# Optimization experiments

Measured on AMD Instinct MI355X. Metric: run time of the kernel, lower is better.

The kernel has to match this reference:

```python
import math
import jax, jax.numpy as jnp
import numpy as np


def setup_inputs() -> dict:
    key = jax.random.key(0)
    k1, k2, k3 = jax.random.split(key, 3)
    n, c, h, w = 4, 128, 64, 64
    return {
        "key": jax.random.normal(k1, (n, c, h, w), dtype=jnp.float32),
        "query": jax.random.normal(k2, (n, c, h, w), dtype=jnp.float32),
        "value": jax.random.normal(k3, (n, c, h, w), dtype=jnp.float32),
    }


def reference(key, query, value):
    n, c, h, w = key.shape
    c2 = value.shape[1]
    hw = h * w
    k = key.reshape(n, c, hw)      # (n, c, hw)
    q = query.reshape(n, c, hw)    # (n, c, hw)
    v = value.reshape(n, c2, hw)   # (n, c2, hw)
    # scores[n, s, t] = sum_c k[n,c,s] * q[n,c,t], scaled by sqrt(c)
    scores = jnp.einsum("ncs,nct->nst", k, q) / math.sqrt(c)
    # softmax over dim=-2 (the key-token axis s)
    p_attn = jax.nn.softmax(scores, axis=-2)
    # p_val[n, e, t] = sum_s v[n,e,s] * p_attn[n,s,t]
    p_val = jnp.einsum("nes,nst->net", v, p_attn)
    return p_val.reshape(n, c2, h, w)
```

## Files before the change

### kernel.cpp

```cpp
#include <hip/hip_runtime.h>


#define HW 4096
#define CC 128
#define KSCALE 0.12751743f
#define CEXP   8.656170245f
#define SMEMB  152576

typedef _Float16 half8  __attribute__((ext_vector_type(8)));
typedef _Float16 half4v __attribute__((ext_vector_type(4)));
typedef float    float4v __attribute__((ext_vector_type(4)));

__device__ __forceinline__ float fast_exp2(float x) {
  return __builtin_amdgcn_exp2f(x);
}

__device__ __forceinline__ void async_copy16(void* lds, const void* g) {
  __builtin_amdgcn_global_load_lds(
      (const __attribute__((address_space(1))) unsigned int*)g,
      (__attribute__((address_space(3))) unsigned int*)lds, 16, 0, 0);
}

__global__ __launch_bounds__(256)
void prepass(const float* __restrict__ K, const float* __restrict__ Q,
             const float* __restrict__ V, _Float16* __restrict__ KT,
             _Float16* __restrict__ QT, _Float16* __restrict__ Vh) {
  const int bid = blockIdx.x;
  const int tid = threadIdx.x;
  if (bid < 2048) {
    __shared__ float tile[32][65];
    const bool isK = bid < 1024;
    const int id = bid & 1023;
    const float* in = isK ? K : Q;
    _Float16* out = isK ? KT : QT;
    const float scale = isK ? KSCALE : 1.0f;
    const int c0 = (id & 3) << 5;
    const int s0 = ((id >> 2) & 63) << 6;
    const int b  = id >> 8;
    const float* ib = in + (size_t)b * CC * HW;
    _Float16* ob = out + (size_t)b * HW * CC;
    const int r  = tid >> 4;
    const int c4 = (tid & 15) * 4;
    *(float4*)&tile[r][c4]      = *(const float4*)(ib + (size_t)(c0 + r) * HW + s0 + c4);
    *(float4*)&tile[r + 16][c4] = *(const float4*)(ib + (size_t)(c0 + r + 16) * HW + s0 + c4);
    __syncthreads();
    const int s  = tid >> 2;
    const int c8 = (tid & 3) * 8;
    half8 h;
    #pragma unroll
    for (int k = 0; k < 8; ++k) h[k] = (_Float16)(tile[c8 + k][s] * scale);
    *(half8*)&ob[(size_t)(s0 + s) * CC + c0 + c8] = h;
  } else {
    const int id = bid - 2048;
    #pragma unroll
    for (int p = 0; p < 4; ++p) {
      const int f = id * 1024 + p * 256 + tid;
      const float4v v = *(const float4v*)(V + 4 * (size_t)f);
      half4v h;
      h.x = (_Float16)v.x; h.y = (_Float16)v.y; h.z = (_Float16)v.z; h.w = (_Float16)v.w;
      *(half4v*)(Vh + 4 * (size_t)f) = h;
    }
  }
}

__global__ __launch_bounds__(512, 4)
void attn_split(const _Float16* __restrict__ KT, const _Float16* __restrict__ QT,
                const _Float16* __restrict__ Vh, float* __restrict__ Opart,
                float* __restrict__ lpart) {
  __shared__ __align__(16) _Float16 sK[2][64][128];
  __shared__ __align__(16) _Float16 sV[2][128][64];
  __shared__ __align__(16) _Float16 sPT[8][16][40];
  __shared__ float sLred[4][2][16];

  const int bid  = blockIdx.x;
  const int xcd  = bid & 7;
  const int idx  = bid >> 3;
  const int half = xcd >> 2;
  const int b    = xcd & 3;
  const int tt0  = idx << 6;
  const int soff = half << 11;
  const int tid  = threadIdx.x;
  const int w    = tid >> 6;
  const int lane = tid & 63;
  const int q    = lane >> 4;
  const int tc   = lane & 15;
  const int g    = w >> 1;
  const int sl   = w & 1;

  const _Float16* KTb = KT + (size_t)b * HW * CC;
  const _Float16* Vb  = Vh + (size_t)b * CC * HW;
  float* Op = Opart + (size_t)(half * 4 + b) * CC * HW;

  half8 qf[4];
  {
    const _Float16* qp = QT + (size_t)b * HW * CC + (size_t)(tt0 + 16 * g + tc) * CC + 8 * q;
    #pragma unroll
    for (int ks = 0; ks < 4; ++ks) qf[ks] = *(const half8*)(qp + 32 * ks);
  }

  const int krow_l = lane >> 4, kchn = lane & 15;
  const int vrow_l = lane >> 3, vchn = lane & 7;
  #define STAGE_S(sn, buf)                                                      \
    {                                                                           \
      _Pragma("unroll")                                                         \
      for (int p = 0; p < 2; ++p) {                                             \
        const int kr = w * 8 + p * 4 + krow_l;                                  \
        const int kg = kchn ^ (kr & 15);                                        \
        async_copy16(&sK[buf][w * 8 + p * 4][0],                                \
                     KTb + (size_t)(soff + (sn) + kr) * CC + kg * 8);           \
        const int vr = w * 16 + p * 8 + vrow_l;                                 \
        const int vg = vchn ^ (vr & 7);                                         \
        async_copy16(&sV[buf][w * 16 + p * 8][0],                               \
                     Vb + (size_t)vr * HW + soff + (sn) + vg * 8);              \
      }                                                                         \
    }

  STAGE_S(0, 0);

  float4v accO[8];
  #pragma unroll
  for (int i2 = 0; i2 < 8; ++i2) accO[i2] = (float4v){0.f, 0.f, 0.f, 0.f};
  float l_part = 0.0f;

  __syncthreads();

  for (int it = 0; it < 2048 / 64; ++it) {
    const int buf = it & 1;
    if (it + 1 < 2048 / 64) STAGE_S((it + 1) * 64, buf ^ 1);

    float4v acc[2];
    acc[0] = (float4v){0.f, 0.f, 0.f, 0.f};
    acc[1] = (float4v){0.f, 0.f, 0.f, 0.f};
    #pragma unroll
    for (int ks = 0; ks < 4; ++ks) {
      #pragma unroll
      for (int j = 0; j < 2; ++j) {
        const int row = 32 * sl + 16 * j + tc;
        const half8 a = *(const half8*)&sK[buf][row][((4 * ks + q) ^ tc) * 8];
        acc[j] = __builtin_amdgcn_mfma_f32_16x16x32_f16(a, qf[ks], acc[j], 0, 0, 0);
      }
    }

    #pragma unroll
    for (int j = 0; j < 2; ++j) {
      const float p0 = fast_exp2(acc[j].x - CEXP);
      const float p1 = fast_exp2(acc[j].y - CEXP);
      const float p2 = fast_exp2(acc[j].z - CEXP);
      const float p3 = fast_exp2(acc[j].w - CEXP);
      l_part += (p0 + p1) + (p2 + p3);
      half4v h;
      h.x = (_Float16)p0; h.y = (_Float16)p1; h.z = (_Float16)p2; h.w = (_Float16)p3;
      *(half4v*)&sPT[w][tc][16 * j + 4 * q] = h;
    }

    const half8 bp = *(const half8*)&sPT[w][tc][8 * q];
    #pragma unroll
    for (int i2 = 0; i2 < 8; ++i2) {
      const half8 av = *(const half8*)&sV[buf][16 * i2 + tc][(((4 * sl + q) ^ (tc & 7))) * 8];
      accO[i2] = __builtin_amdgcn_mfma_f32_16x16x32_f16(av, bp, accO[i2], 0, 0, 0);
    }

    __syncthreads();
  }

  l_part += __shfl_xor(l_part, 16);
  l_part += __shfl_xor(l_part, 32);
  if (lane < 16) sLred[g][sl][tc] = l_part;

  float* mbuf = (float*)&sK[0][0][0];
  if (sl == 1) {
    #pragma unroll
    for (int i2 = 0; i2 < 8; ++i2)
      *(float4v*)&mbuf[g * 2048 + tc * 128 + 16 * i2 + 4 * q] = accO[i2];
  }
  __syncthreads();
  if (sl == 0) {
    const int t = tt0 + 16 * g + tc;
    if (lane < 16) lpart[(size_t)(half * 4 + b) * HW + t] = sLred[g][0][tc] + sLred[g][1][tc];
    #pragma unroll
    for (int i2 = 0; i2 < 8; ++i2) {
      const float4v o = *(const float4v*)&mbuf[g * 2048 + tc * 128 + 16 * i2 + 4 * q];
      const int e0 = 16 * i2 + 4 * q;
      Op[(size_t)(e0 + 0) * HW + t] = accO[i2].x + o.x;
      Op[(size_t)(e0 + 1) * HW + t] = accO[i2].y + o.y;
      Op[(size_t)(e0 + 2) * HW + t] = accO[i2].z + o.z;
      Op[(size_t)(e0 + 3) * HW + t] = accO[i2].w + o.w;
    }
  }
}

__global__ __launch_bounds__(256)
void merge_split(const float* __restrict__ Op, const float* __restrict__ lp,
                 float* __restrict__ out) {
  const int f   = blockIdx.x * 256 + threadIdx.x;
  const int row = f >> 10;
  const int t4  = (f & 1023) << 2;
  const int b   = row >> 7;
  const float4v oa = *(const float4v*)(Op + (size_t)row * HW + t4);
  const float4v ob = *(const float4v*)(Op + ((size_t)row + 512) * HW + t4);
  const float4v la = *(const float4v*)(lp + (size_t)b * HW + t4);
  const float4v lb = *(const float4v*)(lp + ((size_t)b + 4) * HW + t4);
  float4v o;
  o.x = (oa.x + ob.x) / (la.x + lb.x);
  o.y = (oa.y + ob.y) / (la.y + lb.y);
  o.z = (oa.z + ob.z) / (la.z + lb.z);
  o.w = (oa.w + ob.w) / (la.w + lb.w);
  *(float4v*)(out + (size_t)row * HW + t4) = o;
}

__device__ __forceinline__ _Float16* pK(char* s, int buf, int row) {
  return (_Float16*)s + ((size_t)buf * 128 + row) * 128;
}
__device__ __forceinline__ _Float16* pV(char* s, int buf, int row) {
  return (_Float16*)(s + 65536) + ((size_t)buf * 128 + row) * 128;
}
__device__ __forceinline__ _Float16* pP(char* s, int w, int t) {
  return (_Float16*)(s + 131072) + ((size_t)w * 16 + t) * 40;
}
__device__ __forceinline__ float* pL(char* s, int g, int sl) {
  return (float*)(s + 151552) + ((size_t)g * 4 + sl) * 16;
}

__global__ __launch_bounds__(1024, 4)
void attn_mfma(const _Float16* __restrict__ KT, const _Float16* __restrict__ QT,
               const _Float16* __restrict__ Vh, float* __restrict__ Og) {
  __shared__ __align__(16) char smem[SMEMB];
  const int bid = blockIdx.x, tid = threadIdx.x;
  const int b    = bid >> 6;
  const int tt0  = (bid & 63) << 6;
  const int w    = tid >> 6;
  const int lane = tid & 63;
  const int q    = lane >> 4;
  const int tc   = lane & 15;
  const int g    = w >> 2;
  const int sl   = w & 3;

  const _Float16* KTb = KT + (size_t)b * HW * CC;
  const _Float16* Vb  = Vh + (size_t)b * CC * HW;
  float* Ob = Og + (size_t)b * CC * HW;

  half8 qf[4];
  {
    const _Float16* qp = QT + (size_t)b * HW * CC + (size_t)(tt0 + 16 * g + tc) * CC + 8 * q;
    #pragma unroll
    for (int ks = 0; ks < 4; ++ks) qf[ks] = *(const half8*)(qp + 32 * ks);
  }

  const int r0    = w * 8;
  const int lrow  = lane >> 4;
  const int lchnk = lane & 15;
  auto STAGE = [&](int sn, int buf) {
    #pragma unroll
    for (int p = 0; p < 2; ++p) {
      const int row = r0 + p * 4 + lrow;
      const int gc  = lchnk ^ (row & 15);
      async_copy16(pK(smem, buf, r0 + p * 4), KTb + (size_t)(sn + row) * CC + gc * 8);
      async_copy16(pV(smem, buf, r0 + p * 4), Vb + (size_t)row * HW + sn + gc * 8);
    }
  };

  STAGE(0, 0);

  float4v accO[8];
  #pragma unroll
  for (int i2 = 0; i2 < 8; ++i2) accO[i2] = (float4v){0.f, 0.f, 0.f, 0.f};
  float l_part = 0.0f;

  __syncthreads();

  for (int it = 0; it < HW / 128; ++it) {
    const int buf = it & 1;
    if (it + 1 < HW / 128) STAGE((it + 1) * 128, buf ^ 1);

    float4v acc[2];
    acc[0] = (float4v){0.f, 0.f, 0.f, 0.f};
    acc[1] = (float4v){0.f, 0.f, 0.f, 0.f};
    #pragma unroll
    for (int ks = 0; ks < 4; ++ks) {
      #pragma unroll
      for (int j = 0; j < 2; ++j) {
        const int row = 32 * sl + 16 * j + tc;
        const half8 a = *(const half8*)(pK(smem, buf, row) + ((4 * ks + q) ^ tc) * 8);
        acc[j] = __builtin_amdgcn_mfma_f32_16x16x32_f16(a, qf[ks], acc[j], 0, 0, 0);
      }
    }

    #pragma unroll
    for (int j = 0; j < 2; ++j) {
      const float p0 = fast_exp2(acc[j].x - CEXP);
      const float p1 = fast_exp2(acc[j].y - CEXP);
      const float p2 = fast_exp2(acc[j].z - CEXP);
      const float p3 = fast_exp2(acc[j].w - CEXP);
      l_part += (p0 + p1) + (p2 + p3);
      half4v h;
      h.x = (_Float16)p0; h.y = (_Float16)p1; h.z = (_Float16)p2; h.w = (_Float16)p3;
      *(half4v*)(pP(smem, w, tc) + 16 * j + 4 * q) = h;
    }

    const half8 bp = *(const half8*)(pP(smem, w, tc) + 8 * q);
    #pragma unroll
    for (int i2 = 0; i2 < 8; ++i2) {
      const half8 av = *(const half8*)(pV(smem, buf, 16 * i2 + tc) + ((4 * sl + q) ^ tc) * 8);
      accO[i2] = __builtin_amdgcn_mfma_f32_16x16x32_f16(av, bp, accO[i2], 0, 0, 0);
    }

    __syncthreads();
  }

  l_part += __shfl_xor(l_part, 16);
  l_part += __shfl_xor(l_part, 32);
  if (lane < 16) pL(smem, g, sl)[tc] = l_part;

  float* mbuf = (float*)smem;
  if (sl != 0) {
    #pragma unroll
    for (int i2 = 0; i2 < 8; ++i2) {
      const int c4s = (4 * i2 + q) ^ ((tc & 7) << 2);
      *(float4v*)&mbuf[(size_t)(sl - 1) * 8192 + g * 2048 + tc * 128 + 4 * c4s] = accO[i2];
    }
  }
  __syncthreads();
  if (sl == 0) {
    const float li = 1.0f / (((pL(smem, g, 0)[tc] + pL(smem, g, 1)[tc]) +
                              (pL(smem, g, 2)[tc] + pL(smem, g, 3)[tc])));
    const int t = tt0 + 16 * g + tc;
    #pragma unroll
    for (int i2 = 0; i2 < 8; ++i2) {
      const int c4s = (4 * i2 + q) ^ ((tc & 7) << 2);
      float4v o = accO[i2];
      #pragma unroll
      for (int r = 0; r < 3; ++r) {
        const float4v m = *(const float4v*)&mbuf[(size_t)r * 8192 + g * 2048 + tc * 128 + 4 * c4s];
        o.x += m.x; o.y += m.y; o.z += m.z; o.w += m.w;
      }
      const int e0 = 16 * i2 + 4 * q;
      Ob[(size_t)(e0 + 0) * HW + t] = o.x * li;
      Ob[(size_t)(e0 + 1) * HW + t] = o.y * li;
      Ob[(size_t)(e0 + 2) * HW + t] = o.z * li;
      Ob[(size_t)(e0 + 3) * HW + t] = o.w * li;
    }
  }
}

extern "C" void kernel_launch(void* const* d_in, const int* in_sizes, int n_in,
                              void* d_out, int out_size, void* d_ws, size_t ws_size,
                              hipStream_t stream) {
  const float* key   = (const float*)d_in[0];
  const float* query = (const float*)d_in[1];
  const float* value = (const float*)d_in[2];
  float* out = (float*)d_out;

  const size_t TEN   = (size_t)4 * HW * CC * sizeof(_Float16);
  const size_t OPART = (size_t)2 * 4 * CC * HW * sizeof(float);
  const size_t LPART = (size_t)2 * 4 * HW * sizeof(float);
  _Float16* KT = (_Float16*)d_ws;
  _Float16* QT = (_Float16*)((char*)d_ws + TEN);
  _Float16* Vh = (_Float16*)((char*)d_ws + 2 * TEN);
  float* Opart = (float*)((char*)d_ws + 3 * TEN);
  float* lpart = (float*)((char*)d_ws + 3 * TEN + OPART);

  prepass<<<dim3(2560), dim3(256), 0, stream>>>(key, query, value, KT, QT, Vh);
  if (ws_size >= 3 * TEN + OPART + LPART) {
    attn_split<<<dim3(512), dim3(512), 0, stream>>>(KT, QT, Vh, Opart, lpart);
    merge_split<<<dim3(2048), dim3(256), 0, stream>>>(Opart, lpart, out);
  } else {
    attn_mfma<<<dim3(256), dim3(1024), 0, stream>>>(KT, QT, Vh, out);
  }
}
```

Before: 127.8 us.

## Keep attention probabilities in registers and split key rows across waves

Reassigns the wave work split so each wave handles 16 key rows for 32 query tokens, sharing one K fragment across two MFMAs. Exponentiated scores stay in registers and feed a 16x16x16 MFMA directly, which removes the sPT LDS round trip. The cost of this layout is a cross-wave reduction of the output accumulators: partial sums from four waves are combined through staged LDS passes with more barriers. Each wave also holds twice as many accumulator registers, which may limit occupancy.

```diff
diff --git a/kernel.cpp b/kernel.cpp
--- a/kernel.cpp
+++ b/kernel.cpp
@@ -69,8 +69,7 @@
                 float* __restrict__ lpart) {
   __shared__ __align__(16) _Float16 sK[2][64][128];
   __shared__ __align__(16) _Float16 sV[2][128][64];
-  __shared__ __align__(16) _Float16 sPT[8][16][40];
-  __shared__ float sLred[4][2][16];
+  __shared__ float sLred[2][4][32];
 
   const int bid  = blockIdx.x;
   const int xcd  = bid & 7;
@@ -84,18 +83,22 @@
   const int lane = tid & 63;
   const int q    = lane >> 4;
   const int tc   = lane & 15;
-  const int g    = w >> 1;
-  const int sl   = w & 1;
+  const int g2   = w & 1;
+  const int u    = w >> 1;
 
   const _Float16* KTb = KT + (size_t)b * HW * CC;
   const _Float16* Vb  = Vh + (size_t)b * CC * HW;
   float* Op = Opart + (size_t)(half * 4 + b) * CC * HW;
 
-  half8 qf[4];
+  half8 qf[2][4];
   {
-    const _Float16* qp = QT + (size_t)b * HW * CC + (size_t)(tt0 + 16 * g + tc) * CC + 8 * q;
-    #pragma unroll
-    for (int ks = 0; ks < 4; ++ks) qf[ks] = *(const half8*)(qp + 32 * ks);
+    const _Float16* qb = QT + (size_t)b * HW * CC;
+    #pragma unroll
+    for (int f = 0; f < 2; ++f) {
+      const _Float16* qp = qb + (size_t)(tt0 + 32 * g2 + 16 * f + tc) * CC + 8 * q;
+      #pragma unroll
+      for (int ks = 0; ks < 4; ++ks) qf[f][ks] = *(const half8*)(qp + 32 * ks);
+    }
   }
 
   const int krow_l = lane >> 4, kchn = lane & 15;
@@ -117,10 +120,13 @@
 
   STAGE_S(0, 0);
 
-  float4v accO[8];
+  float4v accO[8][2];
   #pragma unroll
-  for (int i2 = 0; i2 < 8; ++i2) accO[i2] = (float4v){0.f, 0.f, 0.f, 0.f};
-  float l_part = 0.0f;
+  for (int i2 = 0; i2 < 8; ++i2) {
+    accO[i2][0] = (float4v){0.f, 0.f, 0.f, 0.f};
+    accO[i2][1] = (float4v){0.f, 0.f, 0.f, 0.f};
+  }
+  float lf0 = 0.0f, lf1 = 0.0f;
 
   __syncthreads();
 
@@ -128,63 +134,95 @@
     const int buf = it & 1;
     if (it + 1 < 2048 / 64) STAGE_S((it + 1) * 64, buf ^ 1);
 
-    float4v acc[2];
-    acc[0] = (float4v){0.f, 0.f, 0.f, 0.f};
-    acc[1] = (float4v){0.f, 0.f, 0.f, 0.f};
+    float4v acc0 = (float4v){0.f, 0.f, 0.f, 0.f};
+    float4v acc1 = (float4v){0.f, 0.f, 0.f, 0.f};
     #pragma unroll
     for (int ks = 0; ks < 4; ++ks) {
-      #pragma unroll
-      for (int j = 0; j < 2; ++j) {
-        const int row = 32 * sl + 16 * j + tc;
-        const half8 a = *(const half8*)&sK[buf][row][((4 * ks + q) ^ tc) * 8];
-        acc[j] = __builtin_amdgcn_mfma_f32_16x16x32_f16(a, qf[ks], acc[j], 0, 0, 0);
-      }
-    }
-
-    #pragma unroll
-    for (int j = 0; j < 2; ++j) {
-      const float p0 = fast_exp2(acc[j].x - CEXP);
-      const float p1 = fast_exp2(acc[j].y - CEXP);
-      const float p2 = fast_exp2(acc[j].z - CEXP);
-      const float p3 = fast_exp2(acc[j].w - CEXP);
-      l_part += (p0 + p1) + (p2 + p3);
-      half4v h;
-      h.x = (_Float16)p0; h.y = (_Float16)p1; h.z = (_Float16)p2; h.w = (_Float16)p3;
-      *(half4v*)&sPT[w][tc][16 * j + 4 * q] = h;
-    }
-
-    const half8 bp = *(const half8*)&sPT[w][tc][8 * q];
+      const half8 a = *(const half8*)&sK[buf][16 * u + tc][((4 * ks + q) ^ tc) * 8];
+      acc0 = __builtin_amdgcn_mfma_f32_16x16x32_f16(a, qf[0][ks], acc0, 0, 0, 0);
+      acc1 = __builtin_amdgcn_mfma_f32_16x16x32_f16(a, qf[1][ks], acc1, 0, 0, 0);
+    }
+
+    half4v pa0, pa1;
+    {
+      const float p0 = fast_exp2(acc0.x - CEXP);
+      const float p1 = fast_exp2(acc0.y - CEXP);
+      const float p2 = fast_exp2(acc0.z - CEXP);
+      const float p3 = fast_exp2(acc0.w - CEXP);
+      lf0 += (p0 + p1) + (p2 + p3);
+      pa0.x = (_Float16)p0; pa0.y = (_Float16)p1; pa0.z = (_Float16)p2; pa0.w = (_Float16)p3;
+    }
+    {
+      const float p0 = fast_exp2(acc1.x - CEXP);
+      const float p1 = fast_exp2(acc1.y - CEXP);
+      const float p2 = fast_exp2(acc1.z - CEXP);
+      const float p3 = fast_exp2(acc1.w - CEXP);
+      lf1 += (p0 + p1) + (p2 + p3);
+      pa1.x = (_Float16)p0; pa1.y = (_Float16)p1; pa1.z = (_Float16)p2; pa1.w = (_Float16)p3;
+    }
+
     #pragma unroll
     for (int i2 = 0; i2 < 8; ++i2) {
-      const half8 av = *(const half8*)&sV[buf][16 * i2 + tc][(((4 * sl + q) ^ (tc & 7))) * 8];
-      accO[i2] = __builtin_amdgcn_mfma_f32_16x16x32_f16(av, bp, accO[i2], 0, 0, 0);
-    }
-
-    __syncthreads();
-  }
-
-  l_part += __shfl_xor(l_part, 16);
-  l_part += __shfl_xor(l_part, 32);
-  if (lane < 16) sLred[g][sl][tc] = l_part;
-
-  float* mbuf = (float*)&sK[0][0][0];
-  if (sl == 1) {
-    #pragma unroll
-    for (int i2 = 0; i2 < 8; ++i2)
-      *(float4v*)&mbuf[g * 2048 + tc * 128 + 16 * i2 + 4 * q] = accO[i2];
-  }
-  __syncthreads();
-  if (sl == 0) {
-    const int t = tt0 + 16 * g + tc;
-    if (lane < 16) lpart[(size_t)(half * 4 + b) * HW + t] = sLred[g][0][tc] + sLred[g][1][tc];
-    #pragma unroll
-    for (int i2 = 0; i2 < 8; ++i2) {
-      const float4v o = *(const float4v*)&mbuf[g * 2048 + tc * 128 + 16 * i2 + 4 * q];
-      const int e0 = 16 * i2 + 4 * q;
-      Op[(size_t)(e0 + 0) * HW + t] = accO[i2].x + o.x;
-      Op[(size_t)(e0 + 1) * HW + t] = accO[i2].y + o.y;
-      Op[(size_t)(e0 + 2) * HW + t] = accO[i2].z + o.z;
-      Op[(size_t)(e0 + 3) * HW + t] = accO[i2].w + o.w;
+      const half4v av = *(const half4v*)
+          &sV[buf][16 * i2 + tc][(((2 * u + (q >> 1)) ^ (tc & 7)) << 3) + ((q & 1) << 2)];
+      accO[i2][0] = __builtin_amdgcn_mfma_f32_16x16x16f16(av, pa0, accO[i2][0], 0, 0, 0);
+      accO[i2][1] = __builtin_amdgcn_mfma_f32_16x16x16f16(av, pa1, accO[i2][1], 0, 0, 0);
+    }
+
+    __syncthreads();
+  }
+
+  lf0 += __shfl_xor(lf0, 16); lf0 += __shfl_xor(lf0, 32);
+  lf1 += __shfl_xor(lf1, 16); lf1 += __shfl_xor(lf1, 32);
+  if (lane < 16) { sLred[g2][u][tc] = lf0; sLred[g2][u][16 + tc] = lf1; }
+
+  float* mb = g2 ? (float*)&sV[0][0][0] : (float*)&sK[0][0][0];
+
+  #pragma unroll
+  for (int f = 0; f < 2; ++f) {
+    __syncthreads();
+    if (u & 1) {
+      float* slot = mb + (u >> 1) * 2112;
+      #pragma unroll
+      for (int i2 = 0; i2 < 8; ++i2)
+        *(float4v*)&slot[tc * 132 + 16 * i2 + 4 * q] = accO[i2][f];
+    }
+    __syncthreads();
+    if (u == 0) {
+      #pragma unroll
+      for (int i2 = 0; i2 < 8; ++i2) {
+        const float4v m = *(const float4v*)&mb[tc * 132 + 16 * i2 + 4 * q];
+        accO[i2][f].x += m.x; accO[i2][f].y += m.y;
+        accO[i2][f].z += m.z; accO[i2][f].w += m.w;
+      }
+    } else if (u == 2) {
+      float* slot = mb + 2112;
+      #pragma unroll
+      for (int i2 = 0; i2 < 8; ++i2) {
+        float4v m = *(const float4v*)&slot[tc * 132 + 16 * i2 + 4 * q];
+        m.x += accO[i2][f].x; m.y += accO[i2][f].y;
+        m.z += accO[i2][f].z; m.w += accO[i2][f].w;
+        *(float4v*)&slot[tc * 132 + 16 * i2 + 4 * q] = m;
+      }
+    }
+    __syncthreads();
+    if (u == 0) {
+      const int t = tt0 + 32 * g2 + 16 * f + tc;
+      if (f == 0 && lane < 32) {
+        const int fl = lane >> 4, tcc = lane & 15;
+        lpart[(size_t)(half * 4 + b) * HW + tt0 + 32 * g2 + 16 * fl + tcc] =
+            (sLred[g2][0][16 * fl + tcc] + sLred[g2][1][16 * fl + tcc]) +
+            (sLred[g2][2][16 * fl + tcc] + sLred[g2][3][16 * fl + tcc]);
+      }
+      #pragma unroll
+      for (int i2 = 0; i2 < 8; ++i2) {
+        const float4v m = *(const float4v*)&mb[2112 + tc * 132 + 16 * i2 + 4 * q];
+        const int e0 = 16 * i2 + 4 * q;
+        Op[(size_t)(e0 + 0) * HW + t] = accO[i2][f].x + m.x;
+        Op[(size_t)(e0 + 1) * HW + t] = accO[i2][f].y + m.y;
+        Op[(size_t)(e0 + 2) * HW + t] = accO[i2][f].z + m.z;
+        Op[(size_t)(e0 + 3) * HW + t] = accO[i2][f].w + m.w;
+      }
     }
   }
 }
```

New measurement: 157.7 us. 23.4% more time.

## Split key axis four ways with smaller tiles and pipelined PV

Applied to the files above, without the earlier changes.

Adds a new attention kernel that splits the key-token axis into four chunks instead of two, launching 1024 blocks with smaller 32-row K/V tiles and 8 blocks per CU occupancy target. The PV matmul for the previous tile is overlapped with the next score computation, and V staging uses a new swizzle. A new merge kernel sums four partials. This aims for more parallelism and occupancy but doubles partial-output traffic to workspace and merge cost.

```diff
diff --git a/kernel.cpp b/kernel.cpp
--- a/kernel.cpp
+++ b/kernel.cpp
@@ -63,6 +63,167 @@
   }
 }
 
+__global__ __launch_bounds__(512, 8)
+void attn_q4(const _Float16* __restrict__ KT, const _Float16* __restrict__ QT,
+             const _Float16* __restrict__ Vh, float* __restrict__ Opart,
+             float* __restrict__ lpart) {
+  __shared__ __align__(16) _Float16 sK[2][32][128];
+  __shared__ __align__(16) _Float16 sV[2][128][32];
+  __shared__ __align__(16) _Float16 sPT[4][16][40];
+  __shared__ float sLred[4][2][16];
+
+  const int bid = blockIdx.x;
+  const int xcd = bid & 7;
+  const int idx = bid >> 3;
+  const int grp = xcd + 8 * (idx >> 6);
+  const int q4  = grp >> 2;
+  const int b   = grp & 3;
+  const int tt0 = (idx & 63) << 6;
+  const int soff = q4 << 10;
+  const int tid  = threadIdx.x;
+  const int w    = tid >> 6;
+  const int lane = tid & 63;
+  const int q    = lane >> 4;
+  const int tc   = lane & 15;
+  const int g    = w >> 1;
+  const int sh   = w & 1;
+
+  const _Float16* KTb = KT + (size_t)b * HW * CC;
+  const _Float16* Vb  = Vh + (size_t)b * CC * HW;
+  float* Op = Opart + (size_t)(q4 * 4 + b) * CC * HW;
+
+  half8 qf[4];
+  {
+    const _Float16* qp = QT + (size_t)b * HW * CC + (size_t)(tt0 + 16 * g + tc) * CC + 8 * q;
+    #pragma unroll
+    for (int ks = 0; ks < 4; ++ks) qf[ks] = *(const half8*)(qp + 32 * ks);
+  }
+
+  const int krow_l = lane >> 4, kchn = lane & 15;
+  const int vrow_l = lane >> 2, vchn = lane & 3;
+  #define STAGE_K(sn, bufn)                                                     \
+    {                                                                           \
+      const int kr = w * 4 + krow_l;                                            \
+      const int kg = kchn ^ (kr & 15);                                          \
+      async_copy16(&sK[bufn][w * 4][0],                                         \
+                   KTb + (size_t)(soff + (sn) + kr) * CC + kg * 8);             \
+    }
+  #define STAGE_V(sn, bufn)                                                     \
+    {                                                                           \
+      const int vr = w * 16 + vrow_l;                                           \
+      const int vg = vchn ^ ((vr & 3) ^ ((vr >> 2) & 3));                       \
+      async_copy16(&sV[bufn][w * 16][0],                                        \
+                   Vb + (size_t)vr * HW + soff + (sn) + vg * 8);                \
+    }
+
+  STAGE_K(0, 0);
+
+  float4v accO[4];
+  #pragma unroll
+  for (int i2 = 0; i2 < 4; ++i2) accO[i2] = (float4v){0.f, 0.f, 0.f, 0.f};
+  float l_part = 0.0f;
+  half4v pcur;
+
+  __syncthreads();
+
+  for (int it = 0; it < 1024 / 32; ++it) {
+    const int buf = it & 1;
+    if (it + 1 < 1024 / 32) STAGE_K((it + 1) * 32, buf ^ 1);
+    STAGE_V(it * 32, buf);
+
+    if (it) {
+      const int pbuf = buf ^ 1;
+      const half8 bp = *(const half8*)&sPT[g][tc][8 * q];
+      __builtin_amdgcn_s_setprio(1);
+      #pragma unroll
+      for (int i2 = 0; i2 < 4; ++i2) {
+        const int e = 64 * sh + 16 * i2 + tc;
+        const half8 av = *(const half8*)
+            &sV[pbuf][e][((q ^ ((e & 3) ^ ((e >> 2) & 3))) * 8)];
+        accO[i2] = __builtin_amdgcn_mfma_f32_16x16x32_f16(av, bp, accO[i2], 0, 0, 0);
+      }
+      __builtin_amdgcn_s_setprio(0);
+    }
+
+    __builtin_amdgcn_sched_barrier(0);
+    __builtin_amdgcn_s_barrier();
+
+    float4v acc = (float4v){0.f, 0.f, 0.f, 0.f};
+    __builtin_amdgcn_s_setprio(1);
+    #pragma unroll
+    for (int ks = 0; ks < 4; ++ks) {
+      const half8 a = *(const half8*)&sK[buf][16 * sh + tc][((4 * ks + q) ^ tc) * 8];
+      acc = __builtin_amdgcn_mfma_f32_16x16x32_f16(a, qf[ks], acc, 0, 0, 0);
+    }
+    __builtin_amdgcn_s_setprio(0);
+
+    {
+      const float p0 = fast_exp2(acc.x - CEXP);
+      const float p1 = fast_exp2(acc.y - CEXP);
+      const float p2 = fast_exp2(acc.z - CEXP);
+      const float p3 = fast_exp2(acc.w - CEXP);
+      l_part += (p0 + p1) + (p2 + p3);
+      half4v h;
+      h.x = (_Float16)p0; h.y = (_Float16)p1; h.z = (_Float16)p2; h.w = (_Float16)p3;
+      *(half4v*)&sPT[g][tc][16 * sh + 4 * q] = h;
+    }
+
+    __syncthreads();
+  }
+
+  {
+    const half8 bp = *(const half8*)&sPT[g][tc][8 * q];
+    __builtin_amdgcn_s_setprio(1);
+    #pragma unroll
+    for (int i2 = 0; i2 < 4; ++i2) {
+      const int e = 64 * sh + 16 * i2 + tc;
+      const half8 av = *(const half8*)
+          &sV[1][e][((q ^ ((e & 3) ^ ((e >> 2) & 3))) * 8)];
+      accO[i2] = __builtin_amdgcn_mfma_f32_16x16x32_f16(av, bp, accO[i2], 0, 0, 0);
+    }
+    __builtin_amdgcn_s_setprio(0);
+  }
+
+  l_part += __shfl_xor(l_part, 16);
+  l_part += __shfl_xor(l_part, 32);
+  if (lane < 16) sLred[g][sh][tc] = l_part;
+  __syncthreads();
+  if (sh == 0 && lane < 16)
+    lpart[(size_t)(q4 * 4 + b) * HW + tt0 + 16 * g + tc] =
+        sLred[g][0][tc] + sLred[g][1][tc];
+
+  const int t = tt0 + 16 * g + tc;
+  #pragma unroll
+  for (int i2 = 0; i2 < 4; ++i2) {
+    const int e0 = 64 * sh + 16 * i2 + 4 * q;
+    Op[(size_t)(e0 + 0) * HW + t] = accO[i2].x;
+    Op[(size_t)(e0 + 1) * HW + t] = accO[i2].y;
+    Op[(size_t)(e0 + 2) * HW + t] = accO[i2].z;
+    Op[(size_t)(e0 + 3) * HW + t] = accO[i2].w;
+  }
+}
+
+__global__ __launch_bounds__(256)
+void merge4(const float* __restrict__ Op, const float* __restrict__ lp,
+            float* __restrict__ out) {
+  const int f   = blockIdx.x * 256 + threadIdx.x;
+  const int row = f >> 10;
+  const int t4  = (f & 1023) << 2;
+  const int b   = row >> 7;
+  float4v o = (float4v){0.f, 0.f, 0.f, 0.f};
+  float4v l = (float4v){0.f, 0.f, 0.f, 0.f};
+  #pragma unroll
+  for (int k = 0; k < 4; ++k) {
+    const float4v ok = *(const float4v*)(Op + ((size_t)k * 512 + row) * HW + t4);
+    const float4v lk = *(const float4v*)(lp + ((size_t)k * 4 + b) * HW + t4);
+    o.x += ok.x; o.y += ok.y; o.z += ok.z; o.w += ok.w;
+    l.x += lk.x; l.y += lk.y; l.z += lk.z; l.w += lk.w;
+  }
+  float4v r;
+  r.x = o.x / l.x; r.y = o.y / l.y; r.z = o.z / l.z; r.w = o.w / l.w;
+  *(float4v*)(out + (size_t)row * HW + t4) = r;
+}
+
 __global__ __launch_bounds__(512, 4)
 void attn_split(const _Float16* __restrict__ KT, const _Float16* __restrict__ QT,
                 const _Float16* __restrict__ Vh, float* __restrict__ Opart,
@@ -100,17 +261,17 @@
 
   const int krow_l = lane >> 4, kchn = lane & 15;
   const int vrow_l = lane >> 3, vchn = lane & 7;
-  #define STAGE_S(sn, buf)                                                      \
+  #define STAGE_S(sn, bufn)                                                     \
     {                                                                           \
       _Pragma("unroll")                                                         \
       for (int p = 0; p < 2; ++p) {                                             \
         const int kr = w * 8 + p * 4 + krow_l;                                  \
         const int kg = kchn ^ (kr & 15);                                        \
-        async_copy16(&sK[buf][w * 8 + p * 4][0],                                \
+        async_copy16(&sK[bufn][w * 8 + p * 4][0],                               \
                      KTb + (size_t)(soff + (sn) + kr) * CC + kg * 8);           \
         const int vr = w * 16 + p * 8 + vrow_l;                                 \
         const int vg = vchn ^ (vr & 7);                                         \
-        async_copy16(&sV[buf][w * 16 + p * 8][0],                               \
+        async_copy16(&sV[bufn][w * 16 + p * 8][0],                              \
                      Vb + (size_t)vr * HW + soff + (sn) + vg * 8);              \
       }                                                                         \
     }
@@ -351,16 +512,22 @@
   float* out = (float*)d_out;
 
   const size_t TEN   = (size_t)4 * HW * CC * sizeof(_Float16);
-  const size_t OPART = (size_t)2 * 4 * CC * HW * sizeof(float);
-  const size_t LPART = (size_t)2 * 4 * HW * sizeof(float);
+  const size_t OP4   = (size_t)4 * 4 * CC * HW * sizeof(float);
+  const size_t LP4   = (size_t)4 * 4 * HW * sizeof(float);
+  const size_t OP2   = (size_t)2 * 4 * CC * HW * sizeof(float);
+  const size_t LP2   = (size_t)2 * 4 * HW * sizeof(float);
   _Float16* KT = (_Float16*)d_ws;
   _Float16* QT = (_Float16*)((char*)d_ws + TEN);
   _Float16* Vh = (_Float16*)((char*)d_ws + 2 * TEN);
   float* Opart = (float*)((char*)d_ws + 3 * TEN);
-  float* lpart = (float*)((char*)d_ws + 3 * TEN + OPART);
 
   prepass<<<dim3(2560), dim3(256), 0, stream>>>(key, query, value, KT, QT, Vh);
-  if (ws_size >= 3 * TEN + OPART + LPART) {
+  if (ws_size >= 3 * TEN + OP4 + LP4) {
+    float* lpart = (float*)((char*)d_ws + 3 * TEN + OP4);
+    attn_q4<<<dim3(1024), dim3(512), 0, stream>>>(KT, QT, Vh, Opart, lpart);
+    merge4<<<dim3(2048), dim3(256), 0, stream>>>(Opart, lpart, out);
+  } else if (ws_size >= 3 * TEN + OP2 + LP2) {
+    float* lpart = (float*)((char*)d_ws + 3 * TEN + OP2);
     attn_split<<<dim3(512), dim3(512), 0, stream>>>(KT, QT, Vh, Opart, lpart);
     merge_split<<<dim3(2048), dim3(256), 0, stream>>>(Opart, lpart, out);
   } else {
```

New measurement: 138.2 us. 1.08x slower.
